# Kernel tuning notes

Hardware: AMD Instinct MI355X
Metric: run time of the kernel (lower is better)

## Reference

```python
import jax, jax.numpy as jnp
import numpy as np

N = 50000
E = 1600000
INPUT_DIM = 128
HEADS = 4
OUT_DIM = 32
LRELU_ALPHA = 0.2


def setup_inputs() -> dict:
    key = jax.random.key(0)
    k1, k2, k3, k4, k5 = jax.random.split(key, 5)
    gain = 1.0 / (1.0 + LRELU_ALPHA)
    input_proj = jax.random.normal(k1, (N, INPUT_DIM), dtype=jnp.float32)
    edge_index = jax.random.randint(k2, (2, E), 0, N, dtype=jnp.int64)
    W = jax.random.normal(k3, (INPUT_DIM, HEADS * OUT_DIM), dtype=jnp.float32) * (gain / INPUT_DIM) ** 0.5
    A_left = jax.random.normal(k4, (HEADS, OUT_DIM, 1), dtype=jnp.float32) * (gain / OUT_DIM)
    A_right = jax.random.normal(k5, (HEADS, OUT_DIM, 1), dtype=jnp.float32) * (gain / OUT_DIM)
    return {"input_proj": input_proj, "edge_index": edge_index, "W": W, "A_left": A_left, "A_right": A_right}


def reference(input_proj, edge_index, W, A_left, A_right):
    n = input_proj.shape[0]
    heads, out_dim = A_left.shape[0], A_left.shape[1]
    # Linear projection: [N, heads, out_dim]
    H = (input_proj @ W).reshape(n, heads, out_dim)
    # Per-node attention scores: [N, heads]
    H_s = jnp.einsum('nhd,hd->nh', H, A_left[..., 0])
    H_t = jnp.einsum('nhd,hd->nh', H, A_right[..., 0])
    src = edge_index[0]
    tgt = edge_index[1]
    # Edge scores: leaky_relu(H_s[src] + H_t[tgt]) -> [E, heads]
    e = H_s[src] + H_t[tgt]
    e = jnp.where(e > 0, e, LRELU_ALPHA * e)
    # Segment softmax over neighborhoods keyed by source node (global max shift, as in original)
    e = jnp.exp(e - jnp.max(e))
    denom = jax.ops.segment_sum(e, src, num_segments=n)  # [N, heads]
    alpha = e / (denom[src] + 1e-8)
    # Weighted scatter-add aggregation of target features: [N, heads, out_dim]
    msg = alpha[:, :, None] * H[tgt]
    agg = jax.ops.segment_sum(msg, src, num_segments=n)
    # concat_last=True -> [N, heads*out_dim], then ELU
    res = agg.reshape(n, heads * out_dim)
    return jax.nn.elu(res)
```

## Files before the change

### kernel.cpp

```cpp
#include <hip/hip_runtime.h>

#define DIM 128
#define HEADS 4
#define ODIM 32
#define LRELU 0.2f
#define PT 4096
#define CAP 9216

typedef unsigned int u32;
typedef unsigned short u16;
typedef unsigned char u8;

typedef __attribute__((ext_vector_type(8))) short bf16x8;
typedef __attribute__((ext_vector_type(4))) float f32x4;

__device__ __forceinline__ u16 f2bf(float f) {
    union { u32 u; float f; } x; x.f = f;
    u32 u = x.u;
    u32 r = u + 0x7FFFu + ((u >> 16) & 1u);
    return (u16)(r >> 16);
}
__device__ __forceinline__ float blo(u32 b) {
    union { u32 u; float f; } x; x.u = b << 16; return x.f;
}
__device__ __forceinline__ float bhi(u32 b) {
    union { u32 u; float f; } x; x.u = b & 0xFFFF0000u; return x.f;
}

__global__ __launch_bounds__(256) void proj_kernel(
    const float* __restrict__ X, const float* __restrict__ W,
    const float* __restrict__ AL, const float* __restrict__ AR,
    u32* __restrict__ Hb, float* __restrict__ Hs, float* __restrict__ Ht,
    int* __restrict__ bcur, int n)
{
    __shared__ alignas(16) u16 sWt[128 * 136];
    __shared__ alignas(16) u16 sXb[64 * 136];
    __shared__ float sAL[DIM], sAR[DIM];
    const int t = threadIdx.x;
    if (blockIdx.x == 0) bcur[t] = t * CAP;
    if (t < DIM) { sAL[t] = AL[t]; sAR[t] = AR[t]; }
    const int row0 = blockIdx.x * 64;

    #pragma unroll
    for (int i = 0; i < 16; ++i) {
        int idx = (i * 256 + t) * 4;
        int k = idx >> 7, nn = idx & 127;
        float4 v = *(const float4*)&W[idx];
        sWt[(nn + 0) * 136 + k] = f2bf(v.x);
        sWt[(nn + 1) * 136 + k] = f2bf(v.y);
        sWt[(nn + 2) * 136 + k] = f2bf(v.z);
        sWt[(nn + 3) * 136 + k] = f2bf(v.w);
    }
    #pragma unroll
    for (int i = 0; i < 8; ++i) {
        int idx = (i * 256 + t) * 4;
        int r = idx >> 7, k = idx & 127;
        int gr = row0 + r;
        float4 v = {0.f, 0.f, 0.f, 0.f};
        if (gr < n) v = *(const float4*)&X[(size_t)gr * DIM + k];
        u16* p = &sXb[r * 136 + k];
        p[0] = f2bf(v.x); p[1] = f2bf(v.y); p[2] = f2bf(v.z); p[3] = f2bf(v.w);
    }
    __syncthreads();

    const int w = t >> 6;
    const int lane = t & 63;
    const int quad = lane >> 4;
    const int nIdx = lane & 15;
    f32x4 acc[8];
    #pragma unroll
    for (int c = 0; c < 8; ++c) acc[c] = (f32x4){0.f, 0.f, 0.f, 0.f};

    const u16* aBase = &sXb[(w * 16 + nIdx) * 136 + quad * 8];
    #pragma unroll
    for (int kq = 0; kq < 4; ++kq) {
        bf16x8 a = *(const bf16x8*)&aBase[kq * 32];
        #pragma unroll
        for (int c = 0; c < 8; ++c) {
            bf16x8 b = *(const bf16x8*)&sWt[(c * 16 + nIdx) * 136 + quad * 8 + kq * 32];
            acc[c] = __builtin_amdgcn_mfma_f32_16x16x32_bf16(a, b, acc[c], 0, 0, 0);
        }
    }
    __syncthreads();
    float* sH = (float*)sWt;
    #pragma unroll
    for (int c = 0; c < 8; ++c)
        #pragma unroll
        for (int r = 0; r < 4; ++r)
            sH[(w * 16 + quad * 4 + r) * 132 + c * 16 + nIdx] = acc[c][r];
    __syncthreads();

    #pragma unroll
    for (int i = 0; i < 16; ++i) {
        int idx = i * 256 + t;
        int r = idx >> 6, d2 = idx & 63;
        int gr = row0 + r;
        if (gr < n) {
            float2 hv = *(const float2*)&sH[r * 132 + 2 * d2];
            Hb[(size_t)gr * 64 + d2] = ((u32)f2bf(hv.y) << 16) | (u32)f2bf(hv.x);
        }
    }
    {
        int r = t >> 2, h = t & 3;
        float s = 0.f, s2 = 0.f;
        #pragma unroll
        for (int q = 0; q < ODIM; q += 4) {
            float4 hv = *(const float4*)&sH[r * 132 + h * ODIM + q];
            s  += hv.x*sAL[h*ODIM+q] + hv.y*sAL[h*ODIM+q+1] + hv.z*sAL[h*ODIM+q+2] + hv.w*sAL[h*ODIM+q+3];
            s2 += hv.x*sAR[h*ODIM+q] + hv.y*sAR[h*ODIM+q+1] + hv.z*sAR[h*ODIM+q+2] + hv.w*sAR[h*ODIM+q+3];
        }
        int gr = row0 + r;
        if (gr < n) { Hs[gr * HEADS + h] = s; Ht[gr * HEADS + h] = s2; }
    }
}

__global__ __launch_bounds__(256) void partition_kernel(
    const int* __restrict__ ei, int* __restrict__ bcur,
    u32* __restrict__ part, int E, int n)
{
    __shared__ u32 stage[PT];
    __shared__ u8  sbkt[PT];
    __shared__ int lcnt[256], loff[256], lcur[256], gbase[256];
    const int t = threadIdx.x;
    const int base = blockIdx.x * PT;
    lcnt[t] = 0;
    __syncthreads();

    u32 key[16];
    int bkt[16];
    #pragma unroll
    for (int i = 0; i < 16; ++i) {
        int e = base + i * 256 + t;
        bkt[i] = -1;
        key[i] = 0;
        if (e < E) {
            int src = ei[e];
            int tgt = ei[E + e];
            src = max(0, min(src, n - 1));
            tgt = max(0, min(tgt, n - 1));
            bkt[i] = src >> 8;
            key[i] = ((u32)(src & 255) << 17) | (u32)tgt;
            atomicAdd(&lcnt[bkt[i]], 1);
        }
    }
    __syncthreads();
    {
        int v = lcnt[t];
        loff[t] = v;
        __syncthreads();
        for (int ofs = 1; ofs < 256; ofs <<= 1) {
            int x = (t >= ofs) ? loff[t - ofs] : 0;
            __syncthreads();
            loff[t] += x;
            __syncthreads();
        }
        int incl = loff[t];
        __syncthreads();
        loff[t] = incl - v;
        lcur[t] = incl - v;
    }
    __syncthreads();
    #pragma unroll
    for (int i = 0; i < 16; ++i) {
        if (bkt[i] >= 0) {
            int p = atomicAdd(&lcur[bkt[i]], 1);
            stage[p] = key[i];
            sbkt[p] = (u8)bkt[i];
        }
    }
    {
        int c = lcnt[t];
        gbase[t] = (c > 0) ? atomicAdd(&bcur[t], c) : 0;
    }
    __syncthreads();
    int total = loff[255] + lcnt[255];
    for (int i = t; i < total; i += 256) {
        int b = sbkt[i];
        int dst = gbase[b] + (i - loff[b]);
        if (dst < (b + 1) * CAP) part[dst] = stage[i];
    }
}

__global__ __launch_bounds__(256) void scanB_kernel(
    const int* __restrict__ bcur, int* __restrict__ tsum,
    int* __restrict__ tpre, int ntiles)
{
    __shared__ int s[256];
    int t = threadIdx.x;
    int cnt = (t < ntiles) ? (bcur[t] - t * CAP) : 0;
    cnt = max(0, min(cnt, CAP));
    s[t] = cnt;
    __syncthreads();
    for (int ofs = 1; ofs < 256; ofs <<= 1) {
        int x = (t >= ofs) ? s[t - ofs] : 0;
        __syncthreads();
        s[t] += x;
        __syncthreads();
    }
    if (t < ntiles) {
        tsum[t] = cnt;
        tpre[t] = s[t] - cnt;
    }
}

__global__ __launch_bounds__(256) void csrfill_kernel(
    const u32* __restrict__ part, const int* __restrict__ tpre,
    const int* __restrict__ tsum, int* __restrict__ off,
    int* __restrict__ csr_tgt, int E, int n, int ntiles)
{
    __shared__ int lc[256], lo[256], lcur[256];
    const int b = blockIdx.x, t = threadIdx.x;
    const int pbase = b * CAP;
    const int base = tpre[b], cnt = tsum[b];
    lc[t] = 0;
    __syncthreads();
    for (int i = t; i < cnt; i += 256)
        atomicAdd(&lc[part[pbase + i] >> 17], 1);
    __syncthreads();
    {
        int v = lc[t];
        lo[t] = v;
        __syncthreads();
        for (int ofs = 1; ofs < 256; ofs <<= 1) {
            int x = (t >= ofs) ? lo[t - ofs] : 0;
            __syncthreads();
            lo[t] += x;
            __syncthreads();
        }
        int incl = lo[t];
        __syncthreads();
        lo[t] = incl - v;
        lcur[t] = incl - v;
    }
    __syncthreads();
    int node = b * 256 + t;
    if (node < n) off[node] = base + lo[t];
    if (b == ntiles - 1 && t == 0) off[n] = base + cnt;
    for (int i = t; i < cnt; i += 256) {
        u32 key = part[pbase + i];
        int p = atomicAdd(&lcur[key >> 17], 1);
        csr_tgt[base + p] = (int)(key & 0x1FFFFu);
    }
}

__global__ __launch_bounds__(256) void agg_kernel(
    const u32* __restrict__ Hb, const float* __restrict__ Hs,
    const float* __restrict__ Ht, const int* __restrict__ off,
    const int* __restrict__ csr_tgt, float2* __restrict__ out, int n, int E)
{
    int node = (blockIdx.x * 256 + threadIdx.x) >> 6;
    int L = threadIdx.x & 63;
    if (node >= n) return;
    int lo = off[node], hi = off[node + 1];
    lo = max(0, min(lo, E));
    hi = max(lo, min(hi, E));
    const int h = L >> 4;
    const int eSel = (L & 31) >> 2;
    const int hSel = L & 3;
    float4 hs4 = *(const float4*)&Hs[node * HEADS];
    float hsC = hSel == 0 ? hs4.x : hSel == 1 ? hs4.y : hSel == 2 ? hs4.z : hs4.w;
    float hsO = h == 0 ? hs4.x : h == 1 ? hs4.y : h == 2 ? hs4.z : hs4.w;
    float ax = 0.f, ay = 0.f, S = 0.f;

    int i = lo;
    for (; i + 8 <= hi; i += 8) {
        int tt[8];
        #pragma unroll
        for (int j = 0; j < 8; ++j) tt[j] = csr_tgt[i + j];
        int tsel = csr_tgt[i + eSel];
        float e = hsC + Ht[tsel * HEADS + hSel];
        float w = __expf(fminf(e > 0.f ? e : LRELU * e, 30.f));
        u32 bb[8];
        #pragma unroll
        for (int j = 0; j < 8; ++j) bb[j] = Hb[tt[j] * 64 + L];
        #pragma unroll
        for (int j = 0; j < 8; ++j) {
            float wj = __shfl(w, (j << 2) | h);
            ax += wj * blo(bb[j]);
            ay += wj * bhi(bb[j]);
            S += wj;
        }
    }
    for (; i < hi; ++i) {
        int tgt = csr_tgt[i];
        float e = hsO + Ht[tgt * HEADS + h];
        float w = __expf(fminf(e > 0.f ? e : LRELU * e, 30.f));
        u32 b = Hb[tgt * 64 + L];
        ax += w * blo(b);
        ay += w * bhi(b);
        S += w;
    }
    float inv = 1.f / (S + 1e-8f);
    float ox = ax * inv, oy = ay * inv;
    ox = ox > 0.f ? ox : (__expf(ox) - 1.f);
    oy = oy > 0.f ? oy : (__expf(oy) - 1.f);
    out[(size_t)node * 64 + L] = {ox, oy};
}

extern "C" void kernel_launch(void* const* d_in, const int* in_sizes, int n_in,
                              void* d_out, int out_size, void* d_ws, size_t ws_size,
                              hipStream_t stream) {
    const float* X  = (const float*)d_in[0];
    const int*   EI = (const int*)d_in[1];
    const float* W  = (const float*)d_in[2];
    const float* AL = (const float*)d_in[3];
    const float* AR = (const float*)d_in[4];
    const int n = in_sizes[0] / DIM;
    const int E = in_sizes[1] / 2;
    const int ntiles = (n + 255) / 256;

    char* ws = (char*)d_ws;
    size_t o = 0;
    auto alloc = [&](size_t bytes) -> void* {
        o = (o + 255) & ~(size_t)255;
        void* p = ws + o;
        o += bytes;
        return p;
    };
    int*   bcur    = (int*)alloc(256 * 4);
    int*   tsum    = (int*)alloc(256 * 4);
    int*   tpre    = (int*)alloc(256 * 4);
    int*   off     = (int*)alloc((size_t)(n + 1) * 4);
    float* Hs      = (float*)alloc((size_t)n * HEADS * 4);
    float* Ht      = (float*)alloc((size_t)n * HEADS * 4);
    int*   csr_tgt = (int*)alloc((size_t)E * 4);
    u32*   part    = (u32*)alloc((size_t)ntiles * CAP * 4);
    u32*   Hb      = (u32*)alloc((size_t)n * 64 * 4);

    proj_kernel<<<(n + 63) / 64, 256, 0, stream>>>(X, W, AL, AR, Hb, Hs, Ht, bcur, n);
    partition_kernel<<<(E + PT - 1) / PT, 256, 0, stream>>>(EI, bcur, part, E, n);
    scanB_kernel<<<1, 256, 0, stream>>>(bcur, tsum, tpre, ntiles);
    csrfill_kernel<<<ntiles, 256, 0, stream>>>(part, tpre, tsum, off, csr_tgt, E, n, ntiles);
    agg_kernel<<<(n + 3) / 4, 256, 0, stream>>>(
        Hb, Hs, Ht, off, csr_tgt, (float2*)d_out, n, E);
}
```

Baseline: 210.7 us.

## Pretranspose W once, load X directly into MFMA, use shuffle scans, drop scan kernel

```diff
diff --git a/kernel.cpp b/kernel.cpp
--- a/kernel.cpp
+++ b/kernel.cpp
@@ -27,62 +27,64 @@
     union { u32 u; float f; } x; x.u = b & 0xFFFF0000u; return x.f;
 }
 
+__global__ __launch_bounds__(256) void prep_kernel(
+    const float* __restrict__ W, u16* __restrict__ Wt, int* __restrict__ bcur)
+{
+    __shared__ u16 s[128 * 136];
+    int t = threadIdx.x;
+    bcur[t] = t * CAP;
+    for (int i = 0; i < 64; ++i) {
+        int idx = i * 256 + t;
+        int k = idx >> 7, nn = idx & 127;
+        s[nn * 136 + k] = f2bf(W[idx]);
+    }
+    __syncthreads();
+    for (int i = 0; i < 64; ++i) {
+        int idx = i * 256 + t;
+        int nn = idx >> 7, k = idx & 127;
+        Wt[idx] = s[nn * 136 + k];
+    }
+}
+
 __global__ __launch_bounds__(256) void proj_kernel(
-    const float* __restrict__ X, const float* __restrict__ W,
+    const float* __restrict__ X, const u16* __restrict__ Wt,
     const float* __restrict__ AL, const float* __restrict__ AR,
-    u32* __restrict__ Hb, float* __restrict__ Hs, float* __restrict__ Ht,
-    int* __restrict__ bcur, int n)
-{
-    __shared__ alignas(16) u16 sWt[128 * 136];
-    __shared__ alignas(16) u16 sXb[64 * 136];
+    u32* __restrict__ Hb, float* __restrict__ Hs, float* __restrict__ Ht, int n)
+{
+    __shared__ alignas(16) float sH[64 * 132];
     __shared__ float sAL[DIM], sAR[DIM];
     const int t = threadIdx.x;
-    if (blockIdx.x == 0) bcur[t] = t * CAP;
     if (t < DIM) { sAL[t] = AL[t]; sAR[t] = AR[t]; }
     const int row0 = blockIdx.x * 64;
-
-    #pragma unroll
-    for (int i = 0; i < 16; ++i) {
-        int idx = (i * 256 + t) * 4;
-        int k = idx >> 7, nn = idx & 127;
-        float4 v = *(const float4*)&W[idx];
-        sWt[(nn + 0) * 136 + k] = f2bf(v.x);
-        sWt[(nn + 1) * 136 + k] = f2bf(v.y);
-        sWt[(nn + 2) * 136 + k] = f2bf(v.z);
-        sWt[(nn + 3) * 136 + k] = f2bf(v.w);
-    }
-    #pragma unroll
-    for (int i = 0; i < 8; ++i) {
-        int idx = (i * 256 + t) * 4;
-        int r = idx >> 7, k = idx & 127;
-        int gr = row0 + r;
-        float4 v = {0.f, 0.f, 0.f, 0.f};
-        if (gr < n) v = *(const float4*)&X[(size_t)gr * DIM + k];
-        u16* p = &sXb[r * 136 + k];
-        p[0] = f2bf(v.x); p[1] = f2bf(v.y); p[2] = f2bf(v.z); p[3] = f2bf(v.w);
-    }
-    __syncthreads();
-
-    const int w = t >> 6;
-    const int lane = t & 63;
-    const int quad = lane >> 4;
-    const int nIdx = lane & 15;
+    const int w = t >> 6, lane = t & 63;
+    const int quad = lane >> 4, nIdx = lane & 15;
+    const int m = row0 + w * 16 + nIdx;
+
     f32x4 acc[8];
     #pragma unroll
     for (int c = 0; c < 8; ++c) acc[c] = (f32x4){0.f, 0.f, 0.f, 0.f};
 
-    const u16* aBase = &sXb[(w * 16 + nIdx) * 136 + quad * 8];
     #pragma unroll
     for (int kq = 0; kq < 4; ++kq) {
-        bf16x8 a = *(const bf16x8*)&aBase[kq * 32];
+        union { bf16x8 v; u16 e[8]; } a;
+        if (m < n) {
+            const float* xp = &X[(size_t)m * DIM + kq * 32 + quad * 8];
+            float4 x0 = *(const float4*)xp;
+            float4 x1 = *(const float4*)(xp + 4);
+            a.e[0] = f2bf(x0.x); a.e[1] = f2bf(x0.y);
+            a.e[2] = f2bf(x0.z); a.e[3] = f2bf(x0.w);
+            a.e[4] = f2bf(x1.x); a.e[5] = f2bf(x1.y);
+            a.e[6] = f2bf(x1.z); a.e[7] = f2bf(x1.w);
+        } else {
+            #pragma unroll
+            for (int j = 0; j < 8; ++j) a.e[j] = 0;
+        }
         #pragma unroll
         for (int c = 0; c < 8; ++c) {
-            bf16x8 b = *(const bf16x8*)&sWt[(c * 16 + nIdx) * 136 + quad * 8 + kq * 32];
-            acc[c] = __builtin_amdgcn_mfma_f32_16x16x32_bf16(a, b, acc[c], 0, 0, 0);
-        }
-    }
-    __syncthreads();
-    float* sH = (float*)sWt;
+            bf16x8 b = *(const bf16x8*)&Wt[(c * 16 + nIdx) * DIM + kq * 32 + quad * 8];
+            acc[c] = __builtin_amdgcn_mfma_f32_16x16x32_bf16(a.v, b, acc[c], 0, 0, 0);
+        }
+    }
     #pragma unroll
     for (int c = 0; c < 8; ++c)
         #pragma unroll
@@ -114,6 +116,23 @@
     }
 }
 
+__device__ __forceinline__ int scan256_excl(int v, int t, int* wsum) {
+    int lane = t & 63, w = t >> 6;
+    int inc = v;
+    #pragma unroll
+    for (int ofs = 1; ofs < 64; ofs <<= 1) {
+        int x = __shfl_up(inc, ofs);
+        if (lane >= ofs) inc += x;
+    }
+    __syncthreads();
+    if (lane == 63) wsum[w] = inc;
+    __syncthreads();
+    int add = 0;
+    #pragma unroll
+    for (int j = 0; j < 4; ++j) add += (j < w) ? wsum[j] : 0;
+    return inc - v + add;
+}
+
 __global__ __launch_bounds__(256) void partition_kernel(
     const int* __restrict__ ei, int* __restrict__ bcur,
     u32* __restrict__ part, int E, int n)
@@ -121,6 +140,7 @@
     __shared__ u32 stage[PT];
     __shared__ u8  sbkt[PT];
     __shared__ int lcnt[256], loff[256], lcur[256], gbase[256];
+    __shared__ int wsum[4];
     const int t = threadIdx.x;
     const int base = blockIdx.x * PT;
     lcnt[t] = 0;
@@ -144,21 +164,11 @@
         }
     }
     __syncthreads();
-    {
-        int v = lcnt[t];
-        loff[t] = v;
-        __syncthreads();
-        for (int ofs = 1; ofs < 256; ofs <<= 1) {
-            int x = (t >= ofs) ? loff[t - ofs] : 0;
-            __syncthreads();
-            loff[t] += x;
-            __syncthreads();
-        }
-        int incl = loff[t];
-        __syncthreads();
-        loff[t] = incl - v;
-        lcur[t] = incl - v;
-    }
+    int cnt = lcnt[t];
+    int ex = scan256_excl(cnt, t, wsum);
+    loff[t] = ex;
+    lcur[t] = ex;
+    gbase[t] = (cnt > 0) ? atomicAdd(&bcur[t], cnt) : 0;
     __syncthreads();
     #pragma unroll
     for (int i = 0; i < 16; ++i) {
@@ -168,10 +178,6 @@
             sbkt[p] = (u8)bkt[i];
         }
     }
-    {
-        int c = lcnt[t];
-        gbase[t] = (c > 0) ? atomicAdd(&bcur[t], c) : 0;
-    }
     __syncthreads();
     int total = loff[255] + lcnt[255];
     for (int i = t; i < total; i += 256) {
@@ -181,57 +187,29 @@
     }
 }
 
-__global__ __launch_bounds__(256) void scanB_kernel(
-    const int* __restrict__ bcur, int* __restrict__ tsum,
-    int* __restrict__ tpre, int ntiles)
-{
-    __shared__ int s[256];
-    int t = threadIdx.x;
-    int cnt = (t < ntiles) ? (bcur[t] - t * CAP) : 0;
-    cnt = max(0, min(cnt, CAP));
-    s[t] = cnt;
-    __syncthreads();
-    for (int ofs = 1; ofs < 256; ofs <<= 1) {
-        int x = (t >= ofs) ? s[t - ofs] : 0;
-        __syncthreads();
-        s[t] += x;
-        __syncthreads();
-    }
-    if (t < ntiles) {
-        tsum[t] = cnt;
-        tpre[t] = s[t] - cnt;
-    }
-}
-
 __global__ __launch_bounds__(256) void csrfill_kernel(
-    const u32* __restrict__ part, const int* __restrict__ tpre,
-    const int* __restrict__ tsum, int* __restrict__ off,
-    int* __restrict__ csr_tgt, int E, int n, int ntiles)
+    const u32* __restrict__ part, const int* __restrict__ bcur,
+    int* __restrict__ off, int* __restrict__ csr_tgt, int n, int ntiles)
 {
     __shared__ int lc[256], lo[256], lcur[256];
+    __shared__ int wsum[4];
+    __shared__ int sBase, sCnt;
     const int b = blockIdx.x, t = threadIdx.x;
+    int myc = (t < ntiles) ? (bcur[t] - t * CAP) : 0;
+    myc = max(0, min(myc, CAP));
+    int ex = scan256_excl(myc, t, wsum);
+    if (t == b) { sBase = ex; sCnt = myc; }
+    lc[t] = 0;
+    __syncthreads();
     const int pbase = b * CAP;
-    const int base = tpre[b], cnt = tsum[b];
-    lc[t] = 0;
-    __syncthreads();
+    const int base = sBase, cnt = sCnt;
     for (int i = t; i < cnt; i += 256)
         atomicAdd(&lc[part[pbase + i] >> 17], 1);
     __syncthreads();
-    {
-        int v = lc[t];
-        lo[t] = v;
-        __syncthreads();
-        for (int ofs = 1; ofs < 256; ofs <<= 1) {
-            int x = (t >= ofs) ? lo[t - ofs] : 0;
-            __syncthreads();
-            lo[t] += x;
-            __syncthreads();
-        }
-        int incl = lo[t];
-        __syncthreads();
-        lo[t] = incl - v;
-        lcur[t] = incl - v;
-    }
+    int v = lc[t];
+    int ex2 = scan256_excl(v, t, wsum);
+    lo[t] = ex2;
+    lcur[t] = ex2;
     __syncthreads();
     int node = b * 256 + t;
     if (node < n) off[node] = base + lo[t];
@@ -318,8 +296,7 @@
         return p;
     };
     int*   bcur    = (int*)alloc(256 * 4);
-    int*   tsum    = (int*)alloc(256 * 4);
-    int*   tpre    = (int*)alloc(256 * 4);
+    u16*   Wt      = (u16*)alloc((size_t)DIM * DIM * 2);
     int*   off     = (int*)alloc((size_t)(n + 1) * 4);
     float* Hs      = (float*)alloc((size_t)n * HEADS * 4);
     float* Ht      = (float*)alloc((size_t)n * HEADS * 4);
@@ -327,10 +304,10 @@
     u32*   part    = (u32*)alloc((size_t)ntiles * CAP * 4);
     u32*   Hb      = (u32*)alloc((size_t)n * 64 * 4);
 
-    proj_kernel<<<(n + 63) / 64, 256, 0, stream>>>(X, W, AL, AR, Hb, Hs, Ht, bcur, n);
+    prep_kernel<<<1, 256, 0, stream>>>(W, Wt, bcur);
+    proj_kernel<<<(n + 63) / 64, 256, 0, stream>>>(X, Wt, AL, AR, Hb, Hs, Ht, n);
     partition_kernel<<<(E + PT - 1) / PT, 256, 0, stream>>>(EI, bcur, part, E, n);
-    scanB_kernel<<<1, 256, 0, stream>>>(bcur, tsum, tpre, ntiles);
-    csrfill_kernel<<<ntiles, 256, 0, stream>>>(part, tpre, tsum, off, csr_tgt, E, n, ntiles);
+    csrfill_kernel<<<ntiles, 256, 0, stream>>>(part, bcur, off, csr_tgt, n, ntiles);
     agg_kernel<<<(n + 3) / 4, 256, 0, stream>>>(
         Hb, Hs, Ht, off, csr_tgt, (float2*)d_out, n, E);
 }
```

Result: no change. 208.3 us (-1.1%).
